# Optimization experiments

Measured on AMD Instinct MI355X. Metric: run time of the kernel, lower is better.

## Reference

```python
import jax, jax.numpy as jnp
import numpy as np

B, S, E = 2, 4096, 512

def setup_inputs() -> dict:
    key = jax.random.key(0)
    kx, kq, kk, kv, ko = jax.random.split(key, 5)
    scale = 1.0 / np.sqrt(E)  # init-style scaling for weights
    return {
        "x": jax.random.normal(kx, (B, S, E), dtype=jnp.float32),
        "Wq": jax.random.normal(kq, (E, E), dtype=jnp.float32) * scale,
        "Wk": jax.random.normal(kk, (E, E), dtype=jnp.float32) * scale,
        "Wv": jax.random.normal(kv, (E, E), dtype=jnp.float32) * scale,
        "Wo": jax.random.normal(ko, (E, E), dtype=jnp.float32) * scale,
        "bo": jnp.zeros((E,), dtype=jnp.float32),
    }

def reference(x, Wq, Wk, Wv, Wo, bo):
    # nn.Linear: y = x @ W.T  (weights stored [out, in])
    q = jnp.einsum("bse,fe->bsf", x, Wq)
    k = jnp.einsum("bse,fe->bsf", x, Wk)
    v = jnp.einsum("bse,fe->bsf", x, Wv)
    inv_scale = 1.0 / jnp.sqrt(jnp.asarray(x.shape[-1], x.dtype))
    scores = jnp.einsum("bqe,bke->bqk", q, k) * inv_scale  # [B,S,S]
    S_len = x.shape[1]
    # torch.triu(ones) keeps j >= i; masked_fill where triu==0 masks j < i
    row = jnp.arange(S_len)[:, None]
    col = jnp.arange(S_len)[None, :]
    keep = col >= row  # [S,S], faithfully anti-causal as in the source
    scores = jnp.where(keep[None, :, :], scores, jnp.asarray(-jnp.inf, scores.dtype))
    attn = jax.nn.softmax(scores, axis=-1)
    # dropout p=0.0 -> identity
    out = jnp.einsum("bqk,bke->bqe", attn, v)
    return jnp.einsum("bse,fe->bsf", out, Wo) + bo
```

## Files before the change

### kernel.cpp

```cpp
#include <hip/hip_runtime.h>
#include <hip/hip_bf16.h>

#define S_LEN 4096
#define E_DIM 512
#define B_DIM 2
#define M_ROWS (B_DIM * S_LEN)

typedef __attribute__((ext_vector_type(8))) short short8;
typedef __attribute__((ext_vector_type(4))) float floatx4;

__device__ __forceinline__ unsigned short f2bf(float f) {
    unsigned u = __float_as_uint(f);
    unsigned r = (u + 0x7fffu + ((u >> 16) & 1u)) >> 16;
    return (unsigned short)r;
}
__device__ __forceinline__ float bf2f(unsigned short u) {
    return __uint_as_float((unsigned)u << 16);
}

__device__ __forceinline__ void async_copy16(unsigned short* lds, const unsigned short* g) {
    auto gp = (const __attribute__((address_space(1))) unsigned int*)g;
    auto lp = (__attribute__((address_space(3))) unsigned int*)lds;
    __builtin_amdgcn_global_load_lds(gp, lp, 16, 0, 0);
}

struct MapArg { unsigned short m[576]; };

__global__ __launch_bounds__(256) void convert_bf16(
    const float* __restrict__ x,  const float* __restrict__ wq,
    const float* __restrict__ wk, const float* __restrict__ wv,
    const float* __restrict__ wo, unsigned short* __restrict__ dstU,
    unsigned short* __restrict__ dstWo)
{
    long i = (long)blockIdx.x * 1024 + (long)threadIdx.x * 4;
    const float* src; long off; unsigned short* dst; long doff;
    if      (i < 4194304) { src = x;  off = i;           dst = dstU;  doff = i; }
    else if (i < 4456448) { src = wq; off = i - 4194304; dst = dstU;  doff = i; }
    else if (i < 4718592) { src = wk; off = i - 4456448; dst = dstU;  doff = i; }
    else if (i < 4980736) { src = wv; off = i - 4718592; dst = dstU;  doff = i; }
    else                  { src = wo; off = i - 4980736; dst = dstWo; doff = i - 4980736; }
    float4 v = *(const float4*)(src + off);
    ushort4 o;
    o.x = f2bf(v.x); o.y = f2bf(v.y); o.z = f2bf(v.z); o.w = f2bf(v.w);
    *(ushort4*)(dst + doff) = o;
}

__device__ __forceinline__ void gemm_core(
    const unsigned short* __restrict__ A, const unsigned short* __restrict__ W,
    void* __restrict__ Cv, const float* __restrict__ bias, int mode,
    int m0, int n0)
{
    __shared__ unsigned short As[128 * 64];
    __shared__ unsigned short Bs[128 * 64];
    const int tid = threadIdx.x;
    const int lane = tid & 63, wave = tid >> 6;
    const int wm = wave >> 1, wn = wave & 1;
    const int q4 = lane >> 4, l16 = lane & 15;
    const int er = l16 & 7;

    floatx4 acc[4][4];
#pragma unroll
    for (int i = 0; i < 4; ++i)
#pragma unroll
        for (int j = 0; j < 4; ++j) acc[i][j] = (floatx4){0.f, 0.f, 0.f, 0.f};

    const int srow = lane >> 3;
    const int scol = ((lane & 7) ^ srow) << 3;

    for (int k0 = 0; k0 < 512; k0 += 64) {
#pragma unroll
        for (int c = 0; c < 4; ++c) {
            const int rbase = c * 32 + wave * 8;
            async_copy16(&As[rbase * 64],
                         A + (size_t)(m0 + rbase + srow) * 512 + k0 + scol);
            async_copy16(&Bs[rbase * 64],
                         W + (size_t)(n0 + rbase + srow) * 512 + k0 + scol);
        }
        __syncthreads();
        short8 af[4][2], bfr[4][2];
        const int c0 = (q4 ^ er) * 8;
#pragma unroll
        for (int i = 0; i < 4; ++i) {
            const int ra = (wm * 64 + i * 16 + l16) * 64;
            const int rb = (wn * 64 + i * 16 + l16) * 64;
            af[i][0]  = *(const short8*)&As[ra + c0];
            af[i][1]  = *(const short8*)&As[ra + (c0 ^ 32)];
            bfr[i][0] = *(const short8*)&Bs[rb + c0];
            bfr[i][1] = *(const short8*)&Bs[rb + (c0 ^ 32)];
        }
#pragma unroll
        for (int h = 0; h < 2; ++h)
#pragma unroll
            for (int i = 0; i < 4; ++i)
#pragma unroll
                for (int j = 0; j < 4; ++j)
                    acc[i][j] = __builtin_amdgcn_mfma_f32_16x16x32_bf16(
                        af[i][h], bfr[j][h], acc[i][j], 0, 0, 0);
        __syncthreads();
    }

    if (mode == 0) {
        unsigned short* C = (unsigned short*)Cv;
#pragma unroll
        for (int i = 0; i < 4; ++i) {
            int rowb = m0 + wm * 64 + i * 16 + q4 * 4;
#pragma unroll
            for (int j = 0; j < 4; ++j) {
                int col = n0 + wn * 64 + j * 16 + l16;
#pragma unroll
                for (int rg = 0; rg < 4; ++rg)
                    C[(size_t)(rowb + rg) * 512 + col] = f2bf(acc[i][j][rg]);
            }
        }
    } else if (mode == 1) {
        unsigned short* C = (unsigned short*)Cv;
#pragma unroll
        for (int i = 0; i < 4; ++i) {
            int grow = m0 + wm * 64 + i * 16 + q4 * 4;
            int b = grow >> 12, s = grow & 4095;
#pragma unroll
            for (int j = 0; j < 4; ++j) {
                int e = n0 + wn * 64 + j * 16 + l16;
                ushort4 pk;
                pk.x = f2bf(acc[i][j][0]); pk.y = f2bf(acc[i][j][1]);
                pk.z = f2bf(acc[i][j][2]); pk.w = f2bf(acc[i][j][3]);
                *(ushort4*)(C + (size_t)b * 512 * 4096 + (size_t)e * 4096 + s) = pk;
            }
        }
    } else {
        float* C = (float*)Cv;
#pragma unroll
        for (int i = 0; i < 4; ++i) {
            int rowb = m0 + wm * 64 + i * 16 + q4 * 4;
#pragma unroll
            for (int j = 0; j < 4; ++j) {
                int col = n0 + wn * 64 + j * 16 + l16;
                float bv = bias[col];
#pragma unroll
                for (int rg = 0; rg < 4; ++rg)
                    C[(size_t)(rowb + rg) * 512 + col] = acc[i][j][rg] + bv;
            }
        }
    }
}

__global__ __launch_bounds__(256) void gemm_qkv(
    const unsigned short* __restrict__ xb,
    const unsigned short* __restrict__ Wqb, const unsigned short* __restrict__ Wkb,
    const unsigned short* __restrict__ Wvb,
    unsigned short* __restrict__ Qb, unsigned short* __restrict__ Kb,
    unsigned short* __restrict__ Vtb)
{
    const int z = blockIdx.z;
    const unsigned short* W = (z == 0) ? Wqb : (z == 1) ? Wkb : Wvb;
    unsigned short* C = (z == 0) ? Qb : (z == 1) ? Kb : Vtb;
    gemm_core(xb, W, C, nullptr, (z == 2) ? 1 : 0, blockIdx.y * 128, blockIdx.x * 128);
}

__global__ __launch_bounds__(256) void gemm_out(
    const unsigned short* __restrict__ AOb, const unsigned short* __restrict__ Wob,
    const float* __restrict__ bo, float* __restrict__ out)
{
    gemm_core(AOb, Wob, out, bo, 2, blockIdx.y * 128, blockIdx.x * 128);
}

__global__ __launch_bounds__(512, 2) void flash_mfma(
    const unsigned short* __restrict__ Qg, const unsigned short* __restrict__ Kg,
    const unsigned short* __restrict__ Vt,
    unsigned short* __restrict__ Oh, float* __restrict__ Lb, MapArg map)
{
    const int enc = map.m[blockIdx.x];
    const int tile = enc & 63, ch = (enc >> 6) & 7, bb = enc >> 9;
    const int i0 = tile * 64;
    const int lo0 = 512 * ch, hi = lo0 + 512;
    const int lo = (i0 > lo0) ? i0 : lo0;
    const int lo_al = lo & ~255;
    const int nsteps = (hi - lo_al) >> 8;

    const int tid = threadIdx.x;
    const int lane = tid & 63, w = tid >> 6;
    const int q4 = lane >> 4, l16 = lane & 15;
    const int e = l16 & 7;
    const float scale = 0.044194173824159216f;
    const float MREF = 4.0f;

    __shared__ unsigned short Qs[64 * 512];
    __shared__ unsigned short Plds[2][64][264];
    __shared__ float Lred[8][64];

    const size_t rowbase = (size_t)bb * S_LEN;
    const size_t vbase   = (size_t)bb * (size_t)512 * 4096;

#pragma unroll
    for (int rr = 0; rr < 8; ++rr) {
        const int row = w * 8 + rr;
        const unsigned short* src = Qg + (rowbase + i0 + row) * 512
                                    + ((lane ^ (row & 7)) << 3);
        async_copy16(&Qs[row * 512], src);
    }

    floatx4 oacc[4][4];
#pragma unroll
    for (int mg = 0; mg < 4; ++mg)
#pragma unroll
        for (int nc = 0; nc < 4; ++nc) oacc[mg][nc] = (floatx4){0.f, 0.f, 0.f, 0.f};
    float l_acc[4] = {0.f, 0.f, 0.f, 0.f};

    const unsigned short* qb0 = &Qs[l16 * 512 + ((q4 ^ e) << 3)];
    const unsigned short* qb1 = &Qs[l16 * 512 + (((q4 + 4) ^ e) << 3)];
    const unsigned short* kpbaseA = Kg + (rowbase + 32 * w + l16) * 512 + (q4 << 3);
    const unsigned short* kpbaseB = kpbaseA + (size_t)16 * 512;
    const unsigned short* vpbase = Vt + vbase + (size_t)(w * 64 + l16) * 4096 + (q4 << 3);

    __syncthreads();

    for (int t = 0; t < nsteps; ++t) {
        const int j0 = lo_al + t * 256;
        const int buf = t & 1;

        short8 kfA[16], kfB[16];
        {
            const unsigned short* kpA = kpbaseA + (size_t)j0 * 512;
            const unsigned short* kpB = kpbaseB + (size_t)j0 * 512;
#pragma unroll
            for (int ks = 0; ks < 16; ++ks) kfA[ks] = *(const short8*)(kpA + ks * 32);
#pragma unroll
            for (int ks = 0; ks < 16; ++ks) kfB[ks] = *(const short8*)(kpB + ks * 32);
        }

        floatx4 sfA[4], sfB[4];
#pragma unroll
        for (int mg = 0; mg < 4; ++mg) {
            sfA[mg] = (floatx4){0.f, 0.f, 0.f, 0.f};
            sfB[mg] = (floatx4){0.f, 0.f, 0.f, 0.f};
        }
        __builtin_amdgcn_s_setprio(1);
#pragma unroll
        for (int ks = 0; ks < 16; ++ks) {
            const unsigned short* qb = (ks & 1) ? qb1 : qb0;
#pragma unroll
            for (int mg = 0; mg < 4; ++mg) {
                short8 a = *(const short8*)(qb + mg * 8192 + (ks >> 1) * 64);
                sfA[mg] = __builtin_amdgcn_mfma_f32_16x16x32_bf16(kfA[ks], a, sfA[mg], 0, 0, 0);
                sfB[mg] = __builtin_amdgcn_mfma_f32_16x16x32_bf16(kfB[ks], a, sfB[mg], 0, 0, 0);
            }
        }
        __builtin_amdgcn_s_setprio(0);

        short8 vc[4], vn[4];
#pragma unroll
        for (int nc = 0; nc < 4; ++nc)
            vc[nc] = *(const short8*)(vpbase + (size_t)(nc * 16) * 4096 + j0);
#pragma unroll
        for (int nc = 0; nc < 4; ++nc)
            vn[nc] = *(const short8*)(vpbase + (size_t)(nc * 16) * 4096 + j0 + 32);

        const int kbA = j0 + 32 * w + (q4 << 2);
        const bool full = (j0 >= i0 + 64);
#pragma unroll
        for (int mg = 0; mg < 4; ++mg) {
            const int row = i0 + mg * 16 + l16;
            float pA0 = __expf(sfA[mg][0] * scale - MREF);
            float pA1 = __expf(sfA[mg][1] * scale - MREF);
            float pA2 = __expf(sfA[mg][2] * scale - MREF);
            float pA3 = __expf(sfA[mg][3] * scale - MREF);
            float pB0 = __expf(sfB[mg][0] * scale - MREF);
            float pB1 = __expf(sfB[mg][1] * scale - MREF);
            float pB2 = __expf(sfB[mg][2] * scale - MREF);
            float pB3 = __expf(sfB[mg][3] * scale - MREF);
            if (!full) {
                pA0 = (kbA + 0 >= row) ? pA0 : 0.f;
                pA1 = (kbA + 1 >= row) ? pA1 : 0.f;
                pA2 = (kbA + 2 >= row) ? pA2 : 0.f;
                pA3 = (kbA + 3 >= row) ? pA3 : 0.f;
                pB0 = (kbA + 16 >= row) ? pB0 : 0.f;
                pB1 = (kbA + 17 >= row) ? pB1 : 0.f;
                pB2 = (kbA + 18 >= row) ? pB2 : 0.f;
                pB3 = (kbA + 19 >= row) ? pB3 : 0.f;
            }
            l_acc[mg] += pA0 + pA1 + pA2 + pA3 + pB0 + pB1 + pB2 + pB3;
            ushort4 pkA, pkB;
            pkA.x = f2bf(pA0); pkA.y = f2bf(pA1); pkA.z = f2bf(pA2); pkA.w = f2bf(pA3);
            pkB.x = f2bf(pB0); pkB.y = f2bf(pB1); pkB.z = f2bf(pB2); pkB.w = f2bf(pB3);
            *(ushort4*)&Plds[buf][mg * 16 + l16][32 * w + (q4 << 2)] = pkA;
            *(ushort4*)&Plds[buf][mg * 16 + l16][32 * w + 16 + (q4 << 2)] = pkB;
        }
        __syncthreads();

        __builtin_amdgcn_s_setprio(1);
#pragma unroll
        for (int kslot = 0; kslot < 8; ++kslot) {
            if (kslot < 7) {
#pragma unroll
                for (int nc = 0; nc < 4; ++nc)
                    vn[nc] = *(const short8*)(vpbase + (size_t)(nc * 16) * 4096
                                              + j0 + (kslot + 1) * 32);
            }
#pragma unroll
            for (int mg = 0; mg < 4; ++mg) {
                short8 ap = *(const short8*)&Plds[buf][mg * 16 + l16][kslot * 32 + (q4 << 3)];
#pragma unroll
                for (int nc = 0; nc < 4; ++nc)
                    oacc[mg][nc] = __builtin_amdgcn_mfma_f32_16x16x32_bf16(
                        ap, vc[nc], oacc[mg][nc], 0, 0, 0);
            }
#pragma unroll
            for (int nc = 0; nc < 4; ++nc) vc[nc] = vn[nc];
        }
        __builtin_amdgcn_s_setprio(0);
    }

#pragma unroll
    for (int mg = 0; mg < 4; ++mg) {
        float v = l_acc[mg];
        v += __shfl_xor(v, 16, 64);
        v += __shfl_xor(v, 32, 64);
        if (q4 == 0) Lred[w][mg * 16 + l16] = v;
    }
    __syncthreads();

    const int slot = 8 * ch * (ch + 1) + bb * 8 * (ch + 1) + tile;
    if (tid < 64) {
        float sum = 0.f;
#pragma unroll
        for (int ww = 0; ww < 8; ++ww) sum += Lred[ww][tid];
        Lb[(size_t)slot * 64 + tid] = sum;
    }

    unsigned short* Op = Oh + (size_t)slot * 64 * 512;
#pragma unroll
    for (int mg = 0; mg < 4; ++mg)
#pragma unroll
        for (int nc = 0; nc < 4; ++nc)
#pragma unroll
            for (int rg = 0; rg < 4; ++rg)
                Op[(size_t)(mg * 16 + q4 * 4 + rg) * 512 + w * 64 + nc * 16 + l16]
                    = f2bf(oacc[mg][nc][rg]);
}

__global__ __launch_bounds__(256) void flash_merge(
    const unsigned short* __restrict__ Oh, const float* __restrict__ Lb,
    unsigned short* __restrict__ AO)
{
    const int row = blockIdx.x * 4 + (threadIdx.x >> 6);
    const int c0 = (threadIdx.x & 63) * 8;
    const int bb = row >> 12, i = row & 4095;
    const int t = i >> 6, ri = i & 63;
    const int chmin = i >> 9;
    float lsum = 0.f;
    float v[8] = {0.f, 0.f, 0.f, 0.f, 0.f, 0.f, 0.f, 0.f};
    for (int ch = chmin; ch < 8; ++ch) {
        int slot = 8 * ch * (ch + 1) + bb * 8 * (ch + 1) + t;
        lsum += Lb[(size_t)slot * 64 + ri];
        short8 p = *(const short8*)(Oh + (size_t)slot * 64 * 512
                                    + (size_t)ri * 512 + c0);
#pragma unroll
        for (int k = 0; k < 8; ++k) v[k] += bf2f((unsigned short)p[k]);
    }
    float inv = 1.f / lsum;
    short8 o;
#pragma unroll
    for (int k = 0; k < 8; ++k) o[k] = (short)f2bf(v[k] * inv);
    *(short8*)(AO + (size_t)row * 512 + c0) = o;
}

static MapArg build_map() {
    MapArg mp{};
    for (int x = 0; x < 8; ++x) {
        const int bb = x >> 2;
        const int chs[2] = {7 - (x & 3), x & 3};
        int enc[72], st[72], n = 0;
        for (int ci = 0; ci < 2; ++ci) {
            const int ch = chs[ci];
            for (int t = 0; t < 8 * (ch + 1); ++t) {
                int i0 = t * 64, lo0 = 512 * ch, hi = lo0 + 512;
                int lo = (i0 > lo0) ? i0 : lo0;
                int lo_al = lo & ~255;
                enc[n] = t | (ch << 6) | (bb << 9);
                st[n] = (hi - lo_al) >> 8;
                ++n;
            }
        }
        for (int i = 1; i < n; ++i) {
            int ev = enc[i], sv = st[i], j = i - 1;
            while (j >= 0 && st[j] < sv) { st[j + 1] = st[j]; enc[j + 1] = enc[j]; --j; }
            st[j + 1] = sv; enc[j + 1] = ev;
        }
        for (int j = 0; j < n; ++j) mp.m[x + 8 * j] = (unsigned short)enc[j];
    }
    return mp;
}

extern "C" void kernel_launch(void* const* d_in, const int* in_sizes, int n_in,
                              void* d_out, int out_size, void* d_ws, size_t ws_size,
                              hipStream_t stream) {
    (void)in_sizes; (void)n_in; (void)out_size; (void)ws_size;
    const float* x  = (const float*)d_in[0];
    const float* Wq = (const float*)d_in[1];
    const float* Wk = (const float*)d_in[2];
    const float* Wv = (const float*)d_in[3];
    const float* Wo = (const float*)d_in[4];
    const float* bo = (const float*)d_in[5];
    float* out = (float*)d_out;

    unsigned short* ws  = (unsigned short*)d_ws;
    unsigned short* Wob = ws;
    unsigned short* QAb = ws + 262144;
    unsigned short* Kb  = QAb + 4194304;
    unsigned short* Vtb = Kb + 4194304;
    unsigned short* U   = Vtb + 4194304;
    unsigned short* xb  = U;
    unsigned short* Wqb = U + 4194304;
    unsigned short* Wkb = Wqb + 262144;
    unsigned short* Wvb = Wkb + 262144;
    unsigned short* Ohb = U;
    float* Lbf = (float*)(U + 18874368);

    static const MapArg mp = build_map();

    convert_bf16<<<5120, 256, 0, stream>>>(x, Wq, Wk, Wv, Wo, U, Wob);

    gemm_qkv<<<dim3(4, 64, 3), 256, 0, stream>>>(xb, Wqb, Wkb, Wvb, QAb, Kb, Vtb);

    flash_mfma<<<576, 512, 0, stream>>>(QAb, Kb, Vtb, Ohb, Lbf, mp);

    flash_merge<<<2048, 256, 0, stream>>>(Ohb, Lbf, QAb);

    gemm_out<<<dim3(4, 64), 256, 0, stream>>>(QAb, Wob, bo, out);
}
```

Measured before the change: 231.7 us.

## Warp-specialize flash kernel into QK/softmax and PV warp groups with pipelined steps

```diff
diff --git a/kernel.cpp b/kernel.cpp
--- a/kernel.cpp
+++ b/kernel.cpp
@@ -174,19 +174,21 @@
     const int i0 = tile * 64;
     const int lo0 = 512 * ch, hi = lo0 + 512;
     const int lo = (i0 > lo0) ? i0 : lo0;
-    const int lo_al = lo & ~255;
-    const int nsteps = (hi - lo_al) >> 8;
+    const int lo_al = lo & ~127;
+    const int nsteps = (hi - lo_al) >> 7;
 
     const int tid = threadIdx.x;
     const int lane = tid & 63, w = tid >> 6;
+    const bool isQK = (w < 4);
+    const int r = w & 3;
     const int q4 = lane >> 4, l16 = lane & 15;
     const int e = l16 & 7;
     const float scale = 0.044194173824159216f;
     const float MREF = 4.0f;
 
     __shared__ unsigned short Qs[64 * 512];
-    __shared__ unsigned short Plds[2][64][264];
-    __shared__ float Lred[8][64];
+    __shared__ unsigned short Plds[2][64][136];
+    __shared__ float Lred[4][64];
 
     const size_t rowbase = (size_t)bb * S_LEN;
     const size_t vbase   = (size_t)bb * (size_t)512 * 4096;
@@ -199,143 +201,142 @@
         async_copy16(&Qs[row * 512], src);
     }
 
-    floatx4 oacc[4][4];
+    floatx4 oacc[4][8];
 #pragma unroll
     for (int mg = 0; mg < 4; ++mg)
 #pragma unroll
-        for (int nc = 0; nc < 4; ++nc) oacc[mg][nc] = (floatx4){0.f, 0.f, 0.f, 0.f};
+        for (int nc = 0; nc < 8; ++nc) oacc[mg][nc] = (floatx4){0.f, 0.f, 0.f, 0.f};
     float l_acc[4] = {0.f, 0.f, 0.f, 0.f};
 
     const unsigned short* qb0 = &Qs[l16 * 512 + ((q4 ^ e) << 3)];
     const unsigned short* qb1 = &Qs[l16 * 512 + (((q4 + 4) ^ e) << 3)];
-    const unsigned short* kpbaseA = Kg + (rowbase + 32 * w + l16) * 512 + (q4 << 3);
+    const unsigned short* kpbaseA = Kg + (rowbase + 32 * r + l16) * 512 + (q4 << 3);
     const unsigned short* kpbaseB = kpbaseA + (size_t)16 * 512;
-    const unsigned short* vpbase = Vt + vbase + (size_t)(w * 64 + l16) * 4096 + (q4 << 3);
+    const unsigned short* vpbase = Vt + vbase + (size_t)(128 * r + l16) * 4096 + (q4 << 3);
 
     __syncthreads();
 
-    for (int t = 0; t < nsteps; ++t) {
-        const int j0 = lo_al + t * 256;
-        const int buf = t & 1;
-
-        short8 kfA[16], kfB[16];
-        {
-            const unsigned short* kpA = kpbaseA + (size_t)j0 * 512;
-            const unsigned short* kpB = kpbaseB + (size_t)j0 * 512;
-#pragma unroll
-            for (int ks = 0; ks < 16; ++ks) kfA[ks] = *(const short8*)(kpA + ks * 32);
-#pragma unroll
-            for (int ks = 0; ks < 16; ++ks) kfB[ks] = *(const short8*)(kpB + ks * 32);
-        }
-
-        floatx4 sfA[4], sfB[4];
+    for (int it = 0; it <= nsteps; ++it) {
+        if (isQK) {
+            if (it < nsteps) {
+                const int j0 = lo_al + it * 128;
+                const unsigned short* kpA = kpbaseA + (size_t)j0 * 512;
+                const unsigned short* kpB = kpbaseB + (size_t)j0 * 512;
+
+                floatx4 sfA[4], sfB[4];
+#pragma unroll
+                for (int mg = 0; mg < 4; ++mg) {
+                    sfA[mg] = (floatx4){0.f, 0.f, 0.f, 0.f};
+                    sfB[mg] = (floatx4){0.f, 0.f, 0.f, 0.f};
+                }
+#pragma unroll
+                for (int g = 0; g < 4; ++g) {
+                    short8 kA[4], kB[4];
+#pragma unroll
+                    for (int k = 0; k < 4; ++k) {
+                        kA[k] = *(const short8*)(kpA + (4 * g + k) * 32);
+                        kB[k] = *(const short8*)(kpB + (4 * g + k) * 32);
+                    }
+#pragma unroll
+                    for (int k = 0; k < 4; ++k) {
+                        const int ks = 4 * g + k;
+                        const unsigned short* qb = (ks & 1) ? qb1 : qb0;
+#pragma unroll
+                        for (int mg = 0; mg < 4; ++mg) {
+                            short8 a = *(const short8*)(qb + mg * 8192 + (ks >> 1) * 64);
+                            sfA[mg] = __builtin_amdgcn_mfma_f32_16x16x32_bf16(kA[k], a, sfA[mg], 0, 0, 0);
+                            sfB[mg] = __builtin_amdgcn_mfma_f32_16x16x32_bf16(kB[k], a, sfB[mg], 0, 0, 0);
+                        }
+                    }
+                }
+
+                const int kbA = j0 + 32 * r + (q4 << 2);
+                const bool full = (j0 >= i0 + 64);
+                const int buf = it & 1;
+#pragma unroll
+                for (int mg = 0; mg < 4; ++mg) {
+                    const int row = i0 + mg * 16 + l16;
+                    float pA0 = __expf(sfA[mg][0] * scale - MREF);
+                    float pA1 = __expf(sfA[mg][1] * scale - MREF);
+                    float pA2 = __expf(sfA[mg][2] * scale - MREF);
+                    float pA3 = __expf(sfA[mg][3] * scale - MREF);
+                    float pB0 = __expf(sfB[mg][0] * scale - MREF);
+                    float pB1 = __expf(sfB[mg][1] * scale - MREF);
+                    float pB2 = __expf(sfB[mg][2] * scale - MREF);
+                    float pB3 = __expf(sfB[mg][3] * scale - MREF);
+                    if (!full) {
+                        pA0 = (kbA + 0 >= row) ? pA0 : 0.f;
+                        pA1 = (kbA + 1 >= row) ? pA1 : 0.f;
+                        pA2 = (kbA + 2 >= row) ? pA2 : 0.f;
+                        pA3 = (kbA + 3 >= row) ? pA3 : 0.f;
+                        pB0 = (kbA + 16 >= row) ? pB0 : 0.f;
+                        pB1 = (kbA + 17 >= row) ? pB1 : 0.f;
+                        pB2 = (kbA + 18 >= row) ? pB2 : 0.f;
+                        pB3 = (kbA + 19 >= row) ? pB3 : 0.f;
+                    }
+                    l_acc[mg] += pA0 + pA1 + pA2 + pA3 + pB0 + pB1 + pB2 + pB3;
+                    ushort4 pkA, pkB;
+                    pkA.x = f2bf(pA0); pkA.y = f2bf(pA1); pkA.z = f2bf(pA2); pkA.w = f2bf(pA3);
+                    pkB.x = f2bf(pB0); pkB.y = f2bf(pB1); pkB.z = f2bf(pB2); pkB.w = f2bf(pB3);
+                    *(ushort4*)&Plds[buf][mg * 16 + l16][32 * r + (q4 << 2)] = pkA;
+                    *(ushort4*)&Plds[buf][mg * 16 + l16][32 * r + 16 + (q4 << 2)] = pkB;
+                }
+            }
+        } else {
+            if (it > 0) {
+                const int j0p = lo_al + (it - 1) * 128;
+                const int buf = (it - 1) & 1;
+#pragma unroll
+                for (int kslot = 0; kslot < 4; ++kslot) {
+                    short8 vf[8];
+#pragma unroll
+                    for (int nc = 0; nc < 8; ++nc)
+                        vf[nc] = *(const short8*)(vpbase + (size_t)(nc * 16) * 4096
+                                                  + j0p + kslot * 32);
+                    short8 ap[4];
+#pragma unroll
+                    for (int mg = 0; mg < 4; ++mg)
+                        ap[mg] = *(const short8*)&Plds[buf][mg * 16 + l16][kslot * 32 + (q4 << 3)];
+#pragma unroll
+                    for (int mg = 0; mg < 4; ++mg)
+#pragma unroll
+                        for (int nc = 0; nc < 8; ++nc)
+                            oacc[mg][nc] = __builtin_amdgcn_mfma_f32_16x16x32_bf16(
+                                ap[mg], vf[nc], oacc[mg][nc], 0, 0, 0);
+                }
+            }
+        }
+        __syncthreads();
+    }
+
+    if (isQK) {
 #pragma unroll
         for (int mg = 0; mg < 4; ++mg) {
-            sfA[mg] = (floatx4){0.f, 0.f, 0.f, 0.f};
-            sfB[mg] = (floatx4){0.f, 0.f, 0.f, 0.f};
-        }
-        __builtin_amdgcn_s_setprio(1);
-#pragma unroll
-        for (int ks = 0; ks < 16; ++ks) {
-            const unsigned short* qb = (ks & 1) ? qb1 : qb0;
-#pragma unroll
-            for (int mg = 0; mg < 4; ++mg) {
-                short8 a = *(const short8*)(qb + mg * 8192 + (ks >> 1) * 64);
-                sfA[mg] = __builtin_amdgcn_mfma_f32_16x16x32_bf16(kfA[ks], a, sfA[mg], 0, 0, 0);
-                sfB[mg] = __builtin_amdgcn_mfma_f32_16x16x32_bf16(kfB[ks], a, sfB[mg], 0, 0, 0);
-            }
-        }
-        __builtin_amdgcn_s_setprio(0);
-
-        short8 vc[4], vn[4];
-#pragma unroll
-        for (int nc = 0; nc < 4; ++nc)
-            vc[nc] = *(const short8*)(vpbase + (size_t)(nc * 16) * 4096 + j0);
-#pragma unroll
-        for (int nc = 0; nc < 4; ++nc)
-            vn[nc] = *(const short8*)(vpbase + (size_t)(nc * 16) * 4096 + j0 + 32);
-
-        const int kbA = j0 + 32 * w + (q4 << 2);
-        const bool full = (j0 >= i0 + 64);
-#pragma unroll
-        for (int mg = 0; mg < 4; ++mg) {
-            const int row = i0 + mg * 16 + l16;
-            float pA0 = __expf(sfA[mg][0] * scale - MREF);
-            float pA1 = __expf(sfA[mg][1] * scale - MREF);
-            float pA2 = __expf(sfA[mg][2] * scale - MREF);
-            float pA3 = __expf(sfA[mg][3] * scale - MREF);
-            float pB0 = __expf(sfB[mg][0] * scale - MREF);
-            float pB1 = __expf(sfB[mg][1] * scale - MREF);
-            float pB2 = __expf(sfB[mg][2] * scale - MREF);
-            float pB3 = __expf(sfB[mg][3] * scale - MREF);
-            if (!full) {
-                pA0 = (kbA + 0 >= row) ? pA0 : 0.f;
-                pA1 = (kbA + 1 >= row) ? pA1 : 0.f;
-                pA2 = (kbA + 2 >= row) ? pA2 : 0.f;
-                pA3 = (kbA + 3 >= row) ? pA3 : 0.f;
-                pB0 = (kbA + 16 >= row) ? pB0 : 0.f;
-                pB1 = (kbA + 17 >= row) ? pB1 : 0.f;
-                pB2 = (kbA + 18 >= row) ? pB2 : 0.f;
-                pB3 = (kbA + 19 >= row) ? pB3 : 0.f;
-            }
-            l_acc[mg] += pA0 + pA1 + pA2 + pA3 + pB0 + pB1 + pB2 + pB3;
-            ushort4 pkA, pkB;
-            pkA.x = f2bf(pA0); pkA.y = f2bf(pA1); pkA.z = f2bf(pA2); pkA.w = f2bf(pA3);
-            pkB.x = f2bf(pB0); pkB.y = f2bf(pB1); pkB.z = f2bf(pB2); pkB.w = f2bf(pB3);
-            *(ushort4*)&Plds[buf][mg * 16 + l16][32 * w + (q4 << 2)] = pkA;
-            *(ushort4*)&Plds[buf][mg * 16 + l16][32 * w + 16 + (q4 << 2)] = pkB;
-        }
-        __syncthreads();
-
-        __builtin_amdgcn_s_setprio(1);
-#pragma unroll
-        for (int kslot = 0; kslot < 8; ++kslot) {
-            if (kslot < 7) {
-#pragma unroll
-                for (int nc = 0; nc < 4; ++nc)
-                    vn[nc] = *(const short8*)(vpbase + (size_t)(nc * 16) * 4096
-                                              + j0 + (kslot + 1) * 32);
-            }
-#pragma unroll
-            for (int mg = 0; mg < 4; ++mg) {
-                short8 ap = *(const short8*)&Plds[buf][mg * 16 + l16][kslot * 32 + (q4 << 3)];
-#pragma unroll
-                for (int nc = 0; nc < 4; ++nc)
-                    oacc[mg][nc] = __builtin_amdgcn_mfma_f32_16x16x32_bf16(
-                        ap, vc[nc], oacc[mg][nc], 0, 0, 0);
-            }
-#pragma unroll
-            for (int nc = 0; nc < 4; ++nc) vc[nc] = vn[nc];
-        }
-        __builtin_amdgcn_s_setprio(0);
-    }
-
-#pragma unroll
-    for (int mg = 0; mg < 4; ++mg) {
-        float v = l_acc[mg];
-        v += __shfl_xor(v, 16, 64);
-        v += __shfl_xor(v, 32, 64);
-        if (q4 == 0) Lred[w][mg * 16 + l16] = v;
+            float v = l_acc[mg];
+            v += __shfl_xor(v, 16, 64);
+            v += __shfl_xor(v, 32, 64);
+            if (q4 == 0) Lred[r][mg * 16 + l16] = v;
+        }
     }
     __syncthreads();
 
     const int slot = 8 * ch * (ch + 1) + bb * 8 * (ch + 1) + tile;
     if (tid < 64) {
-        float sum = 0.f;
-#pragma unroll
-        for (int ww = 0; ww < 8; ++ww) sum += Lred[ww][tid];
+        float sum = Lred[0][tid] + Lred[1][tid] + Lred[2][tid] + Lred[3][tid];
         Lb[(size_t)slot * 64 + tid] = sum;
     }
 
-    unsigned short* Op = Oh + (size_t)slot * 64 * 512;
-#pragma unroll
-    for (int mg = 0; mg < 4; ++mg)
-#pragma unroll
-        for (int nc = 0; nc < 4; ++nc)
-#pragma unroll
-            for (int rg = 0; rg < 4; ++rg)
-                Op[(size_t)(mg * 16 + q4 * 4 + rg) * 512 + w * 64 + nc * 16 + l16]
-                    = f2bf(oacc[mg][nc][rg]);
+    if (!isQK) {
+        unsigned short* Op = Oh + (size_t)slot * 64 * 512;
+#pragma unroll
+        for (int mg = 0; mg < 4; ++mg)
+#pragma unroll
+            for (int nc = 0; nc < 8; ++nc)
+#pragma unroll
+                for (int rg = 0; rg < 4; ++rg)
+                    Op[(size_t)(mg * 16 + q4 * 4 + rg) * 512 + 128 * r + nc * 16 + l16]
+                        = f2bf(oacc[mg][nc][rg]);
+    }
 }
 
 __global__ __launch_bounds__(256) void flash_merge(
@@ -375,9 +376,9 @@
             for (int t = 0; t < 8 * (ch + 1); ++t) {
                 int i0 = t * 64, lo0 = 512 * ch, hi = lo0 + 512;
                 int lo = (i0 > lo0) ? i0 : lo0;
-                int lo_al = lo & ~255;
+                int lo_al = lo & ~127;
                 enc[n] = t | (ch << 6) | (bb << 9);
-                st[n] = (hi - lo_al) >> 8;
+                st[n] = (hi - lo_al) >> 7;
                 ++n;
             }
         }
```

After: 221.4 us. -4.5%, faster.
